# Kernel optimization log

Hardware: AMD Instinct MI355X
Metric: run time of the kernel (lower is better)

Reference implementation:

```python
import jax, jax.numpy as jnp
import numpy as np

B, T, D = 32, 4096, 256
LN_EPS = 1e-5


def setup_inputs() -> dict:
    key = jax.random.key(0)
    k0, k1, k2 = jax.random.split(key, 3)
    byte_ids = jax.random.randint(k0, (B, T), 0, 256, dtype=jnp.int32)
    freq_bands = jnp.ones((D // 2,), jnp.float32)  # nn.Parameter(torch.ones(embed_dim//2))
    # freq_proj: Linear(D, 2D) -> LayerNorm(2D) -> GELU -> Linear(2D, D)
    w1 = jax.random.normal(k1, (D, 2 * D), jnp.float32) * (1.0 / np.sqrt(D))
    b1 = jnp.zeros((2 * D,), jnp.float32)
    gamma = jnp.ones((2 * D,), jnp.float32)
    beta = jnp.zeros((2 * D,), jnp.float32)
    w2 = jax.random.normal(k2, (2 * D, D), jnp.float32) * (1.0 / np.sqrt(2 * D))
    b2 = jnp.zeros((D,), jnp.float32)
    return dict(byte_ids=byte_ids, freq_bands=freq_bands, w1=w1, b1=b1,
                gamma=gamma, beta=beta, w2=w2, b2=b2)


def reference(byte_ids, freq_bands, w1, b1, gamma, beta, w2, b2):
    Bsz, Tlen = byte_ids.shape
    Dm = w1.shape[0]
    k = min(Dm // 2, Tlen // 2)  # static
    signal = byte_ids.astype(jnp.float32) / 127.5 - 1.0  # [B,T]
    # Single FFT; FFT(roll(signal, -pos))[f] == X[f] * exp(+2i*pi*f*pos/T),
    # so |spectrum| is position-invariant and angle shifts linearly in pos.
    X = jnp.fft.fft(signal, axis=1)[:, :k]           # [B,k] complex64
    mag = jnp.abs(X) * freq_bands[:k]                 # [B,k]
    phase0 = jnp.angle(X)                             # [B,k]
    pos = jnp.arange(Tlen, dtype=jnp.float32)
    f = jnp.arange(k, dtype=jnp.float32)
    shift = (2.0 * np.pi / Tlen) * pos[:, None] * f[None, :]      # [T,k]
    phase = phase0[:, None, :] + shift[None, :, :]                 # [B,T,k]
    mag_bt = jnp.broadcast_to(mag[:, None, :], (Bsz, Tlen, k))     # [B,T,k]
    feats = jnp.concatenate([mag_bt, jnp.sin(phase), jnp.cos(phase)], axis=-1)  # [B,T,3k]
    if feats.shape[-1] < Dm:
        feats = jnp.pad(feats, ((0, 0), (0, 0), (0, Dm - feats.shape[-1])))
    else:
        feats = feats[..., :Dm]                        # truncate (drops cos tail)
    # freq_proj MLP
    h = feats @ w1 + b1                                # [B,T,2D]
    mu = jnp.mean(h, axis=-1, keepdims=True)
    var = jnp.var(h, axis=-1, keepdims=True)
    h = (h - mu) * jax.lax.rsqrt(var + LN_EPS) * gamma + beta
    h = jax.nn.gelu(h, approximate=False)              # torch nn.GELU default = exact erf
    return h @ w2 + b2                                 # [B,T,D]
```

## Files before the change

### kernel.cpp

```cpp
#include <hip/hip_runtime.h>


#define T_SZ   4096
#define NFREQ  128

typedef short    bf16x8 __attribute__((ext_vector_type(8)));
typedef unsigned u32x4  __attribute__((ext_vector_type(4)));
typedef float    f32x4  __attribute__((ext_vector_type(4)));

__device__ __forceinline__ float bf2f(unsigned short x) {
  union { unsigned u; float f; } v; v.u = ((unsigned)x) << 16; return v.f;
}
__device__ __forceinline__ float bits2f(unsigned u) {
  union { unsigned u; float f; } v; v.u = u; return v.f;
}
__device__ __forceinline__ unsigned short f2bf(float x) {
  union { float f; unsigned u; } v; v.f = x;
  unsigned r = v.u + 0x7fffu + ((v.u >> 16) & 1u);
  return (unsigned short)(r >> 16);
}
__device__ __forceinline__ unsigned pk2(float lo, float hi) {
  union { float f; unsigned u; } a, b;
  a.f = lo; b.f = hi;
  return __builtin_amdgcn_perm(b.u + 0x8000u, a.u + 0x8000u, 0x07060302u);
}
__device__ __forceinline__ bf16x8 as_bf(u32x4 v) { return __builtin_bit_cast(bf16x8, v); }
__device__ __forceinline__ bool probe_f32(const unsigned* p) {
  return p[0] == 0x3F800000u;
}
__device__ __forceinline__ void stage16(const void* g, const void* lds_base) {
  __builtin_amdgcn_global_load_lds(
      (const __attribute__((address_space(1))) unsigned int*)g,
      (__attribute__((address_space(3))) unsigned int*)lds_base, 16, 0, 0);
}
__device__ __forceinline__ float gelu_f(float v) {
  float u = v * (0.7978845608f + 0.0356774081f * v * v);
  float d = 1.0f + exp2f(-2.885390082f * u);
  return v * __builtin_amdgcn_rcpf(d);
}

__global__ void combo1_kernel(const int* __restrict__ ids,
                              const void* __restrict__ w1, const void* __restrict__ w2,
                              const void* __restrict__ gamma, const void* __restrict__ beta,
                              const void* __restrict__ b2, const void* __restrict__ fb,
                              float2* __restrict__ part,
                              unsigned short* __restrict__ w1sin,
                              unsigned short* __restrict__ w2tp,
                              unsigned short* __restrict__ bia) {
  int bid = blockIdx.x, tid = threadIdx.x;
  if (bid < 2048) {
    int b  = bid >> 6;
    int fg = (bid >> 3) & 7;
    int tp = bid & 7;
    int fl = tid >> 4;
    int m  = tid & 15;
    int f  = fg * 16 + fl;
    const int* row = ids + b * T_SZ + tp * 512;
    const float C = 6.283185307179586f / 4096.0f;
    float re = 0.f, im = 0.f;
    #pragma unroll
    for (int i = 0; i < 8; ++i) {
      int t0 = i * 64 + m * 4;
      int4 iv = *(const int4*)(row + t0);
      int a = ((tp * 512 + t0) * f) & 4095;
#define DFT1(VAL) { float s = (float)(VAL) * (1.0f / 127.5f) - 1.0f;          \
                    float ang = (float)a * C;                                 \
                    re += s * __cosf(ang); im -= s * __sinf(ang);             \
                    a = (a + f) & 4095; }
      DFT1(iv.x) DFT1(iv.y) DFT1(iv.z) DFT1(iv.w)
#undef DFT1
    }
    #pragma unroll
    for (int mask = 1; mask < 16; mask <<= 1) {
      re += __shfl_xor(re, mask, 64);
      im += __shfl_xor(im, mask, 64);
    }
    if (m == 0) part[(tp * 32 + b) * 128 + f] = make_float2(re, im);
    return;
  }
  bool f32 = probe_f32((const unsigned*)fb);
  int id2 = bid - 2048;
  if (id2 < 256) {
    int o = id2 * 256 + tid;
    int f = o & 127, n1 = o >> 7;
    int idx = (128 + f) * 512 + n1;
    w1sin[o] = f32 ? f2bf(((const float*)w1)[idx]) : ((const unsigned short*)w1)[idx];
  } else if (id2 < 768) {
    int o = (id2 - 256) * 256 + tid;
    int p = o & 511, n2 = o >> 9;
    int n1 = ((p >> 5) << 5) | (((p >> 2) & 1) << 4) | (((p >> 3) & 3) << 2) | (p & 3);
    int idx = n1 * 256 + n2;
    w2tp[o] = f32 ? f2bf(((const float*)w2)[idx]) : ((const unsigned short*)w2)[idx];
  } else {
    int i = (id2 - 768) * 256 + tid;
    const void* src; int off;
    if (i < 512)       { src = gamma; off = i; }
    else if (i < 1024) { src = beta;  off = i - 512; }
    else               { src = b2;    off = i - 1024; }
    bia[i] = f32 ? f2bf(((const float*)src)[off]) : ((const unsigned short*)src)[off];
  }
}

__global__ void combo2_kernel(const void* __restrict__ w1, const void* __restrict__ b1,
                              const void* __restrict__ fb,
                              const float2* __restrict__ part,
                              float* __restrict__ ph0,
                              float* __restrict__ hmag) {
  __shared__ float smem[384];
  int bid = blockIdx.x, tid = threadIdx.x;
  bool f32 = probe_f32((const unsigned*)fb);
  if (bid < 16) {
    int idx = bid * 256 + tid;
    int b = idx >> 7, f = idx & 127;
    float re = 0.f, im = 0.f;
    #pragma unroll
    for (int p = 0; p < 8; ++p) {
      float2 v = part[(p * 32 + b) * 128 + f];
      re += v.x; im += v.y;
    }
    ph0[b * NFREQ + f] = atan2f(im, re);
    return;
  }
  int bid2 = bid - 16;
  int b = bid2 >> 3, n1g = bid2 & 7;
  if (tid < 128) {
    int f = tid;
    float re = 0.f, im = 0.f;
    #pragma unroll
    for (int p = 0; p < 8; ++p) {
      float2 v = part[(p * 32 + b) * 128 + f];
      re += v.x; im += v.y;
    }
    float fbv = f32 ? ((const float*)fb)[f] : bf2f(((const unsigned short*)fb)[f]);
    smem[f] = bf2f(f2bf(sqrtf(re * re + im * im) * fbv));
  }
  __syncthreads();
  int fq = tid >> 6, n1l = tid & 63;
  int n1 = n1g * 64 + n1l;
  float acc = 0.f;
  for (int f = fq * 32; f < fq * 32 + 32; ++f) {
    float wv = f32 ? ((const float*)w1)[f * 512 + n1]
                   : bf2f(((const unsigned short*)w1)[f * 512 + n1]);
    acc += smem[f] * bf2f(f2bf(wv));
  }
  smem[128 + tid] = acc;
  __syncthreads();
  if (tid < 64) {
    int n1o = n1g * 64 + tid;
    float a = smem[128 + tid] + smem[192 + tid] + smem[256 + tid] + smem[320 + tid];
    float bv = f32 ? ((const float*)b1)[n1o] : bf2f(((const unsigned short*)b1)[n1o]);
    hmag[b * 512 + n1o] = a + bv;
  }
}

__global__ __launch_bounds__(256, 2)
void fused_kernel(const unsigned short* __restrict__ w1sin,
                  const unsigned short* __restrict__ w2tp,
                  const unsigned short* __restrict__ bias,
                  const float* __restrict__ hmag,
                  const float* __restrict__ ph0,
                  float* __restrict__ out) {
  __shared__ __align__(16) short lds_w[16384];

  const int tid  = threadIdx.x;
  const int wave = tid >> 6;
  const int lane = tid & 63;
  const int quad = lane >> 4;
  const int col  = lane & 15;

  const int blk  = blockIdx.x;
  const int b    = blk >> 5;
  const int my_t = ((blk & 31) << 6) + (wave << 4) + col;

  {
    short* bufp = lds_w;
    #pragma unroll
    for (int i = 0; i < 4; ++i) {
      int rl = wave * 16 + i * 4 + quad;
      int gch = (lane & 15) ^ (rl & 15);
      stage16(w1sin + ((0 * 64 + rl) * 128 + gch * 8), bufp + (wave * 16 + i * 4) * 128);
    }
  }

  u32x4 BsA[4], BsB[4];
  const float* php = ph0 + b * NFREQ;
  const float PHC = 6.283185307179586f / 4096.0f;
  #pragma unroll
  for (int s = 0; s < 4; ++s) {
    u32x4 awA, awB;
    #pragma unroll
    for (int w = 0; w < 4; ++w) {
      int f0 = s * 32 + quad * 8 + w * 2;
      float a0 = __sinf(php[f0]     + (float)((my_t * f0) & 4095) * PHC);
      float a1 = __sinf(php[f0 + 1] + (float)((my_t * (f0 + 1)) & 4095) * PHC);
      awA[w] = pk2(a0, a1);
      awB[w] = awA[w] ^ 0x80000000u;
    }
    BsA[s] = awA; BsB[s] = awB;
  }

  __syncthreads();

  const float* hmagb = hmag + b * 512;
  u32x4 B2A[16], B2B[16];
  float sumA = 0.f, ssqA = 0.f, sumB = 0.f, ssqB = 0.f;
  #pragma unroll
  for (int h = 0; h < 8; ++h) {
    short* cur = lds_w + (h & 1) * 8192;
    short* nxt = lds_w + ((h + 1) & 1) * 8192;
    if (h < 7) {
      #pragma unroll
      for (int i = 0; i < 4; ++i) {
        int rl = wave * 16 + i * 4 + quad;
        int gch = (lane & 15) ^ (rl & 15);
        stage16(w1sin + (((h + 1) * 64 + rl) * 128 + gch * 8),
                nxt + (wave * 16 + i * 4) * 128);
      }
    } else {
      #pragma unroll
      for (int i = 0; i < 4; ++i) {
        int rl = i * 4 + wave;
        int gch = lane ^ (rl & 15);
        stage16(w2tp + ((0 * 16 + rl) * 512 + gch * 8), nxt + rl * 512);
      }
    }
    f32x4 pA = {0.f, 0.f, 0.f, 0.f}, pB = {0.f, 0.f, 0.f, 0.f};
    #pragma unroll
    for (int ntl = 0; ntl < 4; ++ntl) {
      f32x4 aA = *(const f32x4*)(hmagb + h * 64 + ntl * 16 + 4 * quad);
      f32x4 aB = aA;
      #pragma unroll
      for (int s = 0; s < 4; ++s) {
        bf16x8 frag = *(const bf16x8*)(cur + (ntl * 16 + col) * 128
                                           + (((s * 4 + quad) ^ col) << 3));
        aA = __builtin_amdgcn_mfma_f32_16x16x32_bf16(frag, as_bf(BsA[s]), aA, 0, 0, 0);
        aB = __builtin_amdgcn_mfma_f32_16x16x32_bf16(frag, as_bf(BsB[s]), aB, 0, 0, 0);
      }
      #pragma unroll
      for (int jj = 0; jj < 4; ++jj) {
        sumA += aA[jj]; ssqA += aA[jj] * aA[jj];
        sumB += aB[jj]; ssqB += aB[jj] * aB[jj];
      }
      if ((ntl & 1) == 0) { pA = aA; pB = aB; }
      else {
        int s2l = h * 2 + (ntl >> 1);
        u32x4 hA, hB;
        hA[0] = pk2(pA[0], pA[1]); hA[1] = pk2(pA[2], pA[3]);
        hA[2] = pk2(aA[0], aA[1]); hA[3] = pk2(aA[2], aA[3]);
        hB[0] = pk2(pB[0], pB[1]); hB[1] = pk2(pB[2], pB[3]);
        hB[2] = pk2(aB[0], aB[1]); hB[3] = pk2(aB[2], aB[3]);
        B2A[s2l] = hA;
        B2B[s2l] = hB;
      }
    }
    __syncthreads();
  }

  sumA += __shfl_xor(sumA, 16, 64); sumA += __shfl_xor(sumA, 32, 64);
  ssqA += __shfl_xor(ssqA, 16, 64); ssqA += __shfl_xor(ssqA, 32, 64);
  sumB += __shfl_xor(sumB, 16, 64); sumB += __shfl_xor(sumB, 32, 64);
  ssqB += __shfl_xor(ssqB, 16, 64); ssqB += __shfl_xor(ssqB, 32, 64);
  float muA = sumA * (1.0f / 512.0f);
  float varA = fmaxf(ssqA * (1.0f / 512.0f) - muA * muA, 0.0f);
  float rsA = rsqrtf(varA + 1e-5f);
  float muB = sumB * (1.0f / 512.0f);
  float varB = fmaxf(ssqB * (1.0f / 512.0f) - muB * muB, 0.0f);
  float rsB = rsqrtf(varB + 1e-5f);

  const unsigned short* gptr  = bias;
  const unsigned short* beptr = bias + 512;
  #pragma unroll
  for (int s2 = 0; s2 < 16; ++s2) {
    u32x4 hwA = B2A[s2], hwB = B2B[s2], owA, owB;
    #pragma unroll
    for (int w = 0; w < 4; ++w) {
      int nt  = 2 * s2 + (w >> 1);
      int n1b = nt * 16 + 4 * quad + (w & 1) * 2;
      unsigned gp = *(const unsigned*)(gptr + n1b);
      unsigned bp = *(const unsigned*)(beptr + n1b);
      float g0 = bits2f(gp << 16),  g1 = bits2f(gp & 0xffff0000u);
      float e0 = bits2f(bp << 16),  e1 = bits2f(bp & 0xffff0000u);
      float hA0 = bits2f(hwA[w] << 16), hA1 = bits2f(hwA[w] & 0xffff0000u);
      float hB0 = bits2f(hwB[w] << 16), hB1 = bits2f(hwB[w] & 0xffff0000u);
      float tA0 = rsA * g0, tA1 = rsA * g1;
      float tB0 = rsB * g0, tB1 = rsB * g1;
      float vA0 = fmaf(hA0, tA0, fmaf(-muA, tA0, e0));
      float vA1 = fmaf(hA1, tA1, fmaf(-muA, tA1, e1));
      float vB0 = fmaf(hB0, tB0, fmaf(-muB, tB0, e0));
      float vB1 = fmaf(hB1, tB1, fmaf(-muB, tB1, e1));
      owA[w] = pk2(gelu_f(vA0), gelu_f(vA1));
      owB[w] = pk2(gelu_f(vB0), gelu_f(vB1));
    }
    B2A[s2] = owA;
    B2B[s2] = owB;
  }

  const unsigned short* b2p = bias + 1024;
  const long orowA = (long)(b * T_SZ + my_t) * 256;
  const long orowB = orowA + (long)2048 * 256;
  #pragma unroll
  for (int h = 0; h < 16; ++h) {
    short* cur = lds_w + (h & 1) * 8192;
    short* nxt = lds_w + ((h + 1) & 1) * 8192;
    if (h < 15) {
      #pragma unroll
      for (int i = 0; i < 4; ++i) {
        int rl = i * 4 + wave;
        int gch = lane ^ (rl & 15);
        stage16(w2tp + (((h + 1) * 16 + rl) * 512 + gch * 8), nxt + rl * 512);
      }
    }
    f32x4 ccA = {0.f, 0.f, 0.f, 0.f};
    f32x4 ccB = {0.f, 0.f, 0.f, 0.f};
    #pragma unroll
    for (int s2 = 0; s2 < 16; ++s2) {
      bf16x8 A2 = *(const bf16x8*)(cur + col * 512 + (((s2 * 4 + quad) ^ col) << 3));
      ccA = __builtin_amdgcn_mfma_f32_16x16x32_bf16(A2, as_bf(B2A[s2]), ccA, 0, 0, 0);
      ccB = __builtin_amdgcn_mfma_f32_16x16x32_bf16(A2, as_bf(B2B[s2]), ccB, 0, 0, 0);
    }
    unsigned bp0 = *(const unsigned*)(b2p + h * 16 + 4 * quad);
    unsigned bp1 = *(const unsigned*)(b2p + h * 16 + 4 * quad + 2);
    float bb0 = bits2f(bp0 << 16), bb1 = bits2f(bp0 & 0xffff0000u);
    float bb2 = bits2f(bp1 << 16), bb3 = bits2f(bp1 & 0xffff0000u);
    ccA[0] += bb0; ccA[1] += bb1; ccA[2] += bb2; ccA[3] += bb3;
    ccB[0] += bb0; ccB[1] += bb1; ccB[2] += bb2; ccB[3] += bb3;
    *(f32x4*)(out + orowA + h * 16 + quad * 4) = ccA;
    *(f32x4*)(out + orowB + h * 16 + quad * 4) = ccB;
    if (h < 15) __syncthreads();
  }
}

extern "C" void kernel_launch(void* const* d_in, const int* in_sizes, int n_in,
                              void* d_out, int out_size, void* d_ws, size_t ws_size,
                              hipStream_t stream) {
  const int*      ids   = (const int*)d_in[0];
  const void*     fb    = d_in[1];
  const void*     w1    = d_in[2];
  const void*     b1    = d_in[3];
  const void*     gamma = d_in[4];
  const void*     beta  = d_in[5];
  const void*     w2    = d_in[6];
  const void*     b2    = d_in[7];
  float*          out   = (float*)d_out;

  char* ws = (char*)d_ws;
  float*          ph0   = (float*)(ws + 8192);
  unsigned short* bia   = (unsigned short*)(ws + 24576);
  float*          hmag  = (float*)(ws + 32768);
  unsigned short* w1sin = (unsigned short*)(ws + 98304);
  unsigned short* w2tp  = (unsigned short*)(ws + 229376);
  float2*         part  = (float2*)(ws + 491520);

  combo1_kernel<<<dim3(2821), dim3(256), 0, stream>>>(ids, w1, w2, gamma, beta, b2, fb,
                                                      part, w1sin, w2tp, bia);
  combo2_kernel<<<dim3(272), dim3(256), 0, stream>>>(w1, b1, fb, part, ph0, hmag);
  fused_kernel<<<dim3(1024), dim3(256), 0, stream>>>(w1sin, w2tp, bia, hmag, ph0, out);
}
```

Measured before the change: 225.9 us.

## Fold spectrum reduction and magnitude projection into fused kernel, drop combo2 launch

Removes the separate combo2 kernel and has every fused_kernel block recompute its batch's phase, magnitude and the magnitude-times-W1 projection (128x512) into shared memory. This eliminates one kernel launch and the global round-trip for hmag/ph0. In exchange, each of the 32 blocks per batch redundantly does the 128-step projection, reading 256KB of W1 per block and adding latency before the main MFMA loop.

```diff
diff --git a/kernel.cpp b/kernel.cpp
--- a/kernel.cpp
+++ b/kernel.cpp
@@ -101,66 +101,19 @@
   }
 }
 
-__global__ void combo2_kernel(const void* __restrict__ w1, const void* __restrict__ b1,
-                              const void* __restrict__ fb,
-                              const float2* __restrict__ part,
-                              float* __restrict__ ph0,
-                              float* __restrict__ hmag) {
-  __shared__ float smem[384];
-  int bid = blockIdx.x, tid = threadIdx.x;
-  bool f32 = probe_f32((const unsigned*)fb);
-  if (bid < 16) {
-    int idx = bid * 256 + tid;
-    int b = idx >> 7, f = idx & 127;
-    float re = 0.f, im = 0.f;
-    #pragma unroll
-    for (int p = 0; p < 8; ++p) {
-      float2 v = part[(p * 32 + b) * 128 + f];
-      re += v.x; im += v.y;
-    }
-    ph0[b * NFREQ + f] = atan2f(im, re);
-    return;
-  }
-  int bid2 = bid - 16;
-  int b = bid2 >> 3, n1g = bid2 & 7;
-  if (tid < 128) {
-    int f = tid;
-    float re = 0.f, im = 0.f;
-    #pragma unroll
-    for (int p = 0; p < 8; ++p) {
-      float2 v = part[(p * 32 + b) * 128 + f];
-      re += v.x; im += v.y;
-    }
-    float fbv = f32 ? ((const float*)fb)[f] : bf2f(((const unsigned short*)fb)[f]);
-    smem[f] = bf2f(f2bf(sqrtf(re * re + im * im) * fbv));
-  }
-  __syncthreads();
-  int fq = tid >> 6, n1l = tid & 63;
-  int n1 = n1g * 64 + n1l;
-  float acc = 0.f;
-  for (int f = fq * 32; f < fq * 32 + 32; ++f) {
-    float wv = f32 ? ((const float*)w1)[f * 512 + n1]
-                   : bf2f(((const unsigned short*)w1)[f * 512 + n1]);
-    acc += smem[f] * bf2f(f2bf(wv));
-  }
-  smem[128 + tid] = acc;
-  __syncthreads();
-  if (tid < 64) {
-    int n1o = n1g * 64 + tid;
-    float a = smem[128 + tid] + smem[192 + tid] + smem[256 + tid] + smem[320 + tid];
-    float bv = f32 ? ((const float*)b1)[n1o] : bf2f(((const unsigned short*)b1)[n1o]);
-    hmag[b * 512 + n1o] = a + bv;
-  }
-}
-
 __global__ __launch_bounds__(256, 2)
 void fused_kernel(const unsigned short* __restrict__ w1sin,
                   const unsigned short* __restrict__ w2tp,
                   const unsigned short* __restrict__ bias,
-                  const float* __restrict__ hmag,
-                  const float* __restrict__ ph0,
+                  const void* __restrict__ w1,
+                  const void* __restrict__ b1,
+                  const void* __restrict__ fb,
+                  const float2* __restrict__ part,
                   float* __restrict__ out) {
   __shared__ __align__(16) short lds_w[16384];
+  __shared__ __align__(16) float s_hmag[512];
+  __shared__ float s_ph0[128];
+  __shared__ float s_mag[128];
 
   const int tid  = threadIdx.x;
   const int wave = tid >> 6;
@@ -182,8 +135,47 @@
     }
   }
 
+  const bool f32w = probe_f32((const unsigned*)fb);
+
+  if (tid < 128) {
+    int f = tid;
+    float re = 0.f, im = 0.f;
+    #pragma unroll
+    for (int p = 0; p < 8; ++p) {
+      float2 v = part[(p * 32 + b) * 128 + f];
+      re += v.x; im += v.y;
+    }
+    float fbv = f32w ? ((const float*)fb)[f] : bf2f(((const unsigned short*)fb)[f]);
+    s_mag[f] = bf2f(f2bf(sqrtf(re * re + im * im) * fbv));
+    s_ph0[f] = atan2f(im, re);
+  }
+  __syncthreads();
+
+  {
+    float acc0 = 0.f, acc1 = 0.f;
+    const int n1a = tid, n1c = tid + 256;
+    if (f32w) {
+      const float* w1f = (const float*)w1;
+      for (int f = 0; f < 128; ++f) {
+        float mg = s_mag[f];
+        acc0 += mg * bf2f(f2bf(w1f[f * 512 + n1a]));
+        acc1 += mg * bf2f(f2bf(w1f[f * 512 + n1c]));
+      }
+    } else {
+      const unsigned short* w1h = (const unsigned short*)w1;
+      for (int f = 0; f < 128; ++f) {
+        float mg = s_mag[f];
+        acc0 += mg * bf2f(f2bf(bf2f(w1h[f * 512 + n1a])));
+        acc1 += mg * bf2f(f2bf(bf2f(w1h[f * 512 + n1c])));
+      }
+    }
+    float bv0 = f32w ? ((const float*)b1)[n1a] : bf2f(((const unsigned short*)b1)[n1a]);
+    float bv1 = f32w ? ((const float*)b1)[n1c] : bf2f(((const unsigned short*)b1)[n1c]);
+    s_hmag[n1a] = acc0 + bv0;
+    s_hmag[n1c] = acc1 + bv1;
+  }
+
   u32x4 BsA[4], BsB[4];
-  const float* php = ph0 + b * NFREQ;
   const float PHC = 6.283185307179586f / 4096.0f;
   #pragma unroll
   for (int s = 0; s < 4; ++s) {
@@ -191,8 +183,8 @@
     #pragma unroll
     for (int w = 0; w < 4; ++w) {
       int f0 = s * 32 + quad * 8 + w * 2;
-      float a0 = __sinf(php[f0]     + (float)((my_t * f0) & 4095) * PHC);
-      float a1 = __sinf(php[f0 + 1] + (float)((my_t * (f0 + 1)) & 4095) * PHC);
+      float a0 = __sinf(s_ph0[f0]     + (float)((my_t * f0) & 4095) * PHC);
+      float a1 = __sinf(s_ph0[f0 + 1] + (float)((my_t * (f0 + 1)) & 4095) * PHC);
       awA[w] = pk2(a0, a1);
       awB[w] = awA[w] ^ 0x80000000u;
     }
@@ -201,7 +193,6 @@
 
   __syncthreads();
 
-  const float* hmagb = hmag + b * 512;
   u32x4 B2A[16], B2B[16];
   float sumA = 0.f, ssqA = 0.f, sumB = 0.f, ssqB = 0.f;
   #pragma unroll
@@ -227,7 +218,7 @@
     f32x4 pA = {0.f, 0.f, 0.f, 0.f}, pB = {0.f, 0.f, 0.f, 0.f};
     #pragma unroll
     for (int ntl = 0; ntl < 4; ++ntl) {
-      f32x4 aA = *(const f32x4*)(hmagb + h * 64 + ntl * 16 + 4 * quad);
+      f32x4 aA = *(const f32x4*)(s_hmag + h * 64 + ntl * 16 + 4 * quad);
       f32x4 aB = aA;
       #pragma unroll
       for (int s = 0; s < 4; ++s) {
@@ -344,15 +335,13 @@
   float*          out   = (float*)d_out;
 
   char* ws = (char*)d_ws;
-  float*          ph0   = (float*)(ws + 8192);
   unsigned short* bia   = (unsigned short*)(ws + 24576);
-  float*          hmag  = (float*)(ws + 32768);
   unsigned short* w1sin = (unsigned short*)(ws + 98304);
   unsigned short* w2tp  = (unsigned short*)(ws + 229376);
   float2*         part  = (float2*)(ws + 491520);
 
   combo1_kernel<<<dim3(2821), dim3(256), 0, stream>>>(ids, w1, w2, gamma, beta, b2, fb,
                                                       part, w1sin, w2tp, bia);
-  combo2_kernel<<<dim3(272), dim3(256), 0, stream>>>(w1, b1, fb, part, ph0, hmag);
-  fused_kernel<<<dim3(1024), dim3(256), 0, stream>>>(w1sin, w2tp, bia, hmag, ph0, out);
-}
+  fused_kernel<<<dim3(1024), dim3(256), 0, stream>>>(w1sin, w2tp, bia, w1, b1, fb,
+                                                     part, out);
+}
```

Result: slower. 257.3 us (+13.9%).
